# Performance work log

Measured on AMD Instinct MI355X. Metric: run time of the kernel, lower is better.

## Reference

```python
import jax, jax.numpy as jnp
import numpy as np

K = 2            # top-k experts
SCALING = 16.0 / 16.0  # alpha / r


def setup_inputs() -> dict:
    key = jax.random.key(0)
    ks = jax.random.split(key, 7)
    B, T, D, O, E, R = 2, 4096, 2048, 2048, 8, 16
    return {
        "x": jax.random.normal(ks[0], (B, T, D), dtype=jnp.float32),
        "W": jax.random.normal(ks[1], (O, D), dtype=jnp.float32) * (1.0 / np.sqrt(D)),
        "b": jax.random.normal(ks[2], (O,), dtype=jnp.float32) * 0.02,
        "lora_A": jax.random.normal(ks[3], (E, R, D), dtype=jnp.float32) * (1.0 / np.sqrt(D)),
        "lora_B": jax.random.normal(ks[4], (E, O, R), dtype=jnp.float32) * 0.02,
        "gate_w": jax.random.normal(ks[5], (E, D), dtype=jnp.float32) * 0.02,
        "gate_b": jax.random.normal(ks[6], (E,), dtype=jnp.float32) * 0.02,
    }


def reference(x, W, b, lora_A, lora_B, gate_w, gate_b):
    orig_shape = x.shape
    D = orig_shape[-1]
    O = W.shape[0]
    x_flat = x.reshape(-1, D)                                  # [N, D]

    base = x_flat @ W.T + b                                    # [N, O]

    logits = x_flat @ gate_w.T + gate_b                        # [N, E] (eval: no noise)
    topk_logits, topk_idx = jax.lax.top_k(logits, K)           # [N, K]
    gates = jax.nn.softmax(topk_logits, axis=-1)               # [N, K]

    xA = jnp.einsum('nd,erd->ner', x_flat, lora_A)             # [N, E, R]
    delta_all = jnp.einsum('ner,eor->neo', xA, lora_B)         # [N, E, O]

    delta_topk = jnp.take_along_axis(delta_all, topk_idx[:, :, None], axis=1)  # [N, K, O]
    lora_update = jnp.sum(delta_topk * gates[:, :, None], axis=1)              # [N, O]

    out = base + SCALING * lora_update
    return out.reshape(*orig_shape[:-1], O)
```

## Files before the change

### kernel.cpp

```cpp
#include <hip/hip_runtime.h>
#include <hip/hip_bf16.h>
#include <stdint.h>

#define N_ROWS 8192
#define DIM    2048
#define OUTD   2048
#define NEXP   8
#define RNK    16
#define ZCOLS  128
#define KAUG   2176

typedef unsigned short u16;
typedef float  f32x4  __attribute__((ext_vector_type(4)));
typedef __bf16 bf16x8 __attribute__((ext_vector_type(8)));

__device__ __forceinline__ u16 f2bf(float f) {
  unsigned u = __float_as_uint(f);
  return (u16)((u + 0x7fffu + ((u >> 16) & 1u)) >> 16);
}

__global__ __launch_bounds__(256) void k2_weights(
    const float* __restrict__ W, const float* __restrict__ lB,
    const float* __restrict__ lA, u16* __restrict__ waug, u16* __restrict__ ab)
{
  const int t = threadIdx.x;
  const int bid = blockIdx.x;
  if (bid < OUTD) {
    const int o = bid;
    const float* wr = W + (size_t)o * DIM;
    u16* dst = waug + (size_t)o * KAUG;
    #pragma unroll
    for (int i = 0; i < 2; ++i) {
      int c = t * 4 + i * 1024;
      float4 v = *(const float4*)(wr + c);
      ushort4 s; s.x = f2bf(v.x); s.y = f2bf(v.y); s.z = f2bf(v.z); s.w = f2bf(v.w);
      *(ushort4*)(dst + c) = s;
    }
    if (t < ZCOLS) {
      int e = t >> 4, r = t & 15;
      dst[DIM + t] = f2bf(lB[((size_t)e * OUTD + o) * RNK + r]);
    }
  } else {
    const int ar = bid - OUTD;
    const float* src = lA + (size_t)ar * DIM;
    u16* dst = ab + (size_t)ar * DIM;
    #pragma unroll
    for (int i = 0; i < 2; ++i) {
      int c = t * 4 + i * 1024;
      float4 v = *(const float4*)(src + c);
      ushort4 s; s.x = f2bf(v.x); s.y = f2bf(v.y); s.z = f2bf(v.z); s.w = f2bf(v.w);
      *(ushort4*)(dst + c) = s;
    }
  }
}

__global__ __launch_bounds__(256) void kf_fused(
    const float* __restrict__ x, const float* __restrict__ gw,
    const float* __restrict__ gb, const u16* __restrict__ ab,
    u16* __restrict__ xaug)
{
  __shared__ __align__(16) u16 la[8192];
  __shared__ __align__(16) u16 xb[1024];
  __shared__ float4 gates[16];

  const int t    = threadIdx.x;
  const int wave = t >> 6;
  const int lane = t & 63;
  const int r    = t >> 4;
  const int q    = t & 15;
  const size_t row0 = (size_t)blockIdx.x * 16;

  int   lrow[4], lsch[4];
  #pragma unroll
  for (int i = 0; i < 4; ++i) {
    const int g = t + i * 256;
    lrow[i] = g >> 3;
    lsch[i] = (g & 7) ^ (lrow[i] & 7);
  }

  float4 xv, gwv[8];
  xv = *(const float4*)(x + (row0 + r) * DIM + q * 4);
  #pragma unroll
  for (int e = 0; e < NEXP; ++e)
    gwv[e] = *(const float4*)(gw + (size_t)e * DIM + q * 4);

  float ga[NEXP] = {};
  f32x4 acc[2] = {};
  const int nfA = 2 * wave, nfB = 2 * wave + 1;

  for (int c = 0; c < 32; ++c) {
    const int C0 = c * 64;
    #pragma unroll
    for (int i = 0; i < 4; ++i) {
      const char* src = (const char*)(ab + (size_t)lrow[i] * DIM + C0 + lsch[i] * 8);
      __builtin_amdgcn_global_load_lds(
          (__attribute__((address_space(1))) void*)src,
          (__attribute__((address_space(3))) void*)((char*)la + (wave * 64 + i * 256) * 16),
          16, 0, 0);
    }
    __builtin_amdgcn_sched_barrier(0);
    float4 xvn, gwvn[8];
    if (c + 1 < 32) {
      xvn = *(const float4*)(x + (row0 + r) * DIM + C0 + 64 + q * 4);
      #pragma unroll
      for (int e = 0; e < NEXP; ++e)
        gwvn[e] = *(const float4*)(gw + (size_t)e * DIM + C0 + 64 + q * 4);
    }
    __builtin_amdgcn_sched_barrier(0);
    ushort4 s; s.x = f2bf(xv.x); s.y = f2bf(xv.y); s.z = f2bf(xv.z); s.w = f2bf(xv.w);
    *(ushort4*)(xaug + (row0 + r) * KAUG + C0 + q * 4) = s;
    #pragma unroll
    for (int e = 0; e < NEXP; ++e)
      ga[e] += xv.x * gwv[e].x + xv.y * gwv[e].y + xv.z * gwv[e].z + xv.w * gwv[e].w;
    {
      const int ch = q >> 1;
      const int by = r * 128 + ((ch ^ (r & 7)) * 16) + (q & 1) * 8;
      *(ushort4*)((char*)xb + by) = s;
    }
    if (c + 1 < 32) asm volatile("s_waitcnt vmcnt(9)" ::: "memory");
    else            asm volatile("s_waitcnt vmcnt(0)" ::: "memory");
    asm volatile("s_waitcnt lgkmcnt(0)" ::: "memory");
    __builtin_amdgcn_s_barrier();

    #pragma unroll
    for (int ks = 0; ks < 2; ++ks) {
      const int ra  = lane & 15;
      const int pa  = ((ks * 4 + (lane >> 4)) ^ (ra & 7)) * 16;
      bf16x8 avf = *(const bf16x8*)((char*)xb + ra * 128 + pa);
      const int rbA = (lane & 15) + 16 * nfA;
      const int rbB = (lane & 15) + 16 * nfB;
      bf16x8 bvA = *(const bf16x8*)((char*)la + rbA * 128 + (((ks * 4 + (lane >> 4)) ^ (rbA & 7)) * 16));
      bf16x8 bvB = *(const bf16x8*)((char*)la + rbB * 128 + (((ks * 4 + (lane >> 4)) ^ (rbB & 7)) * 16));
      acc[0] = __builtin_amdgcn_mfma_f32_16x16x32_bf16(avf, bvA, acc[0], 0, 0, 0);
      acc[1] = __builtin_amdgcn_mfma_f32_16x16x32_bf16(avf, bvB, acc[1], 0, 0, 0);
    }
    __builtin_amdgcn_s_barrier();
    xv = xvn;
    #pragma unroll
    for (int e = 0; e < NEXP; ++e) gwv[e] = gwvn[e];
  }

  #pragma unroll
  for (int e = 0; e < NEXP; ++e) {
    float v = ga[e];
    v += __shfl_xor(v, 1); v += __shfl_xor(v, 2);
    v += __shfl_xor(v, 4); v += __shfl_xor(v, 8);
    ga[e] = v + gb[e];
  }
  if (q == 0) {
    int e0 = 0; float m0 = ga[0];
    #pragma unroll
    for (int e = 1; e < NEXP; ++e) if (ga[e] > m0) { m0 = ga[e]; e0 = e; }
    int e1 = (e0 == 0) ? 1 : 0; float m1 = ga[e1];
    #pragma unroll
    for (int e = 0; e < NEXP; ++e) if (e != e0 && ga[e] > m1) { m1 = ga[e]; e1 = e; }
    float tt  = expf(m1 - m0);
    float inv = 1.f / (1.f + tt);
    float4 gg; gg.x = inv; gg.y = tt * inv;
    gg.z = __int_as_float(e0); gg.w = __int_as_float(e1);
    gates[r] = gg;
  }
  __syncthreads();

  #pragma unroll
  for (int nfl = 0; nfl < 2; ++nfl) {
    const int e = 2 * wave + nfl;
    const int n = e * 16 + (lane & 15);
    #pragma unroll
    for (int j = 0; j < 4; ++j) {
      const int m = (lane >> 4) * 4 + j;
      float4 gg = gates[m];
      const float g = (e == __float_as_int(gg.z)) ? gg.x
                    : ((e == __float_as_int(gg.w)) ? gg.y : 0.f);
      xaug[(row0 + m) * KAUG + DIM + n] = f2bf(acc[nfl][j] * g);
    }
  }
}

__global__ __launch_bounds__(512, 2) void gemm256_pipe(
    const u16* __restrict__ A, int lda,
    const u16* __restrict__ Bm, int ldb,
    int Ksz, int grid_n,
    float* __restrict__ outF, int ldo, const float* __restrict__ bias)
{
  __shared__ __align__(16) u16 smem[65536];

  const int tid  = threadIdx.x;
  const int wave = tid >> 6;
  const int lane = tid & 63;

  int bid = blockIdx.x;
  const int nwg = gridDim.x;
  if ((nwg & 7) == 0) {
    const int cpx = nwg >> 3;
    bid = (bid & 7) * cpx + (bid >> 3);
  }
  const int tm = bid / grid_n;
  const int tn = bid % grid_n;
  const size_t row0 = (size_t)tm * 256;
  const size_t col0 = (size_t)tn * 256;

  const int l3  = lane >> 3;
  const int sch = ((lane & 7) ^ l3) << 4;
  const char* aSrc = (const char*)(A  + (row0 + (size_t)(wave * 8 + l3)) * lda) + sch;
  const char* bSrc = (const char*)(Bm + (col0 + (size_t)(wave * 8 + l3)) * ldb) + sch;
  const size_t arst = (size_t)lda * 128;
  const size_t brst = (size_t)ldb * 128;
  char* ldsA = (char*)smem + wave * 1024;
  char* ldsB = (char*)smem + 65536 + wave * 1024;

  auto stage = [&](int tt) {
    const size_t ko = (size_t)tt * 128;
    const int    sb = (tt & 1) << 15;
    #pragma unroll
    for (int i = 0; i < 4; ++i)
      __builtin_amdgcn_global_load_lds(
          (__attribute__((address_space(1))) void*)(aSrc + ko + i * arst),
          (__attribute__((address_space(3))) void*)(ldsA + sb + i * 8192), 16, 0, 0);
    #pragma unroll
    for (int i = 0; i < 4; ++i)
      __builtin_amdgcn_global_load_lds(
          (__attribute__((address_space(1))) void*)(bSrc + ko + i * brst),
          (__attribute__((address_space(3))) void*)(ldsB + sb + i * 8192), 16, 0, 0);
  };

  const int wm = wave >> 2, wn = wave & 3;
  const int x0 = ((lane >> 4) ^ (lane & 7)) << 4;
  const int offA0 = wm * 16384 + (lane & 15) * 128 + x0;
  const int offB0 = wn * 8192  + (lane & 15) * 128 + x0;

  f32x4 acc[8][4] = {};

  const int nk = Ksz / 64;
  stage(0); stage(1);

  for (int t = 0; t < nk; ++t) {
    if (t + 1 < nk) asm volatile("s_waitcnt vmcnt(8)" ::: "memory");
    else            asm volatile("s_waitcnt vmcnt(0)" ::: "memory");
    __builtin_amdgcn_s_barrier();
    __builtin_amdgcn_sched_barrier(0);

    const char* sa = (const char*)smem + ((t & 1) << 15);
    const char* sb = (const char*)smem + 65536 + ((t & 1) << 15);

    bf16x8 av0[8], bv0[4], av1[8], bv1[4];
    #pragma unroll
    for (int mf = 0; mf < 8; ++mf) av0[mf] = *(const bf16x8*)(sa + offA0 + mf * 2048);
    #pragma unroll
    for (int nf = 0; nf < 4; ++nf) bv0[nf] = *(const bf16x8*)(sb + offB0 + nf * 2048);
    __builtin_amdgcn_s_setprio(1);
    #pragma unroll
    for (int mf = 0; mf < 8; ++mf)
      #pragma unroll
      for (int nf = 0; nf < 2; ++nf)
        acc[mf][nf] = __builtin_amdgcn_mfma_f32_16x16x32_bf16(
            av0[mf], bv0[nf], acc[mf][nf], 0, 0, 0);
    __builtin_amdgcn_s_setprio(0);
    #pragma unroll
    for (int mf = 0; mf < 8; ++mf) av1[mf] = *(const bf16x8*)(sa + (offA0 ^ 64) + mf * 2048);
    #pragma unroll
    for (int nf = 0; nf < 4; ++nf) bv1[nf] = *(const bf16x8*)(sb + (offB0 ^ 64) + nf * 2048);
    __builtin_amdgcn_s_setprio(1);
    #pragma unroll
    for (int mf = 0; mf < 8; ++mf)
      #pragma unroll
      for (int nf = 2; nf < 4; ++nf)
        acc[mf][nf] = __builtin_amdgcn_mfma_f32_16x16x32_bf16(
            av0[mf], bv0[nf], acc[mf][nf], 0, 0, 0);
    __builtin_amdgcn_s_setprio(0);
    asm volatile("s_waitcnt lgkmcnt(0)" ::: "memory");
    __builtin_amdgcn_s_barrier();
    __builtin_amdgcn_sched_barrier(0);
    if (t + 2 < nk) stage(t + 2);
    __builtin_amdgcn_s_setprio(1);
    #pragma unroll
    for (int mf = 0; mf < 8; ++mf)
      #pragma unroll
      for (int nf = 0; nf < 4; ++nf)
        acc[mf][nf] = __builtin_amdgcn_mfma_f32_16x16x32_bf16(
            av1[mf], bv1[nf], acc[mf][nf], 0, 0, 0);
    __builtin_amdgcn_s_setprio(0);
  }

  #pragma unroll
  for (int nf = 0; nf < 4; ++nf) {
    const size_t c = col0 + wn * 64 + nf * 16 + (lane & 15);
    const float bvv = bias[c];
    #pragma unroll
    for (int mf = 0; mf < 8; ++mf) {
      const size_t rb = row0 + wm * 128 + mf * 16 + ((lane >> 4) << 2);
      #pragma unroll
      for (int j = 0; j < 4; ++j)
        outF[(rb + j) * (size_t)ldo + c] = acc[mf][nf][j] + bvv;
    }
  }
}

extern "C" void kernel_launch(void* const* d_in, const int* in_sizes, int n_in,
                              void* d_out, int out_size, void* d_ws, size_t ws_size,
                              hipStream_t stream) {
  const float* x  = (const float*)d_in[0];
  const float* W  = (const float*)d_in[1];
  const float* b  = (const float*)d_in[2];
  const float* lA = (const float*)d_in[3];
  const float* lB = (const float*)d_in[4];
  const float* gw = (const float*)d_in[5];
  const float* gb = (const float*)d_in[6];
  float* out = (float*)d_out;

  u16* xaug = (u16*)d_ws;
  u16* waug = xaug + (size_t)N_ROWS * KAUG;
  u16* ab   = waug + (size_t)OUTD * KAUG;

  hipLaunchKernelGGL(k2_weights, dim3(OUTD + ZCOLS), dim3(256), 0, stream,
                     W, lB, lA, waug, ab);
  hipLaunchKernelGGL(kf_fused, dim3(N_ROWS / 16), dim3(256), 0, stream,
                     x, gw, gb, ab, xaug);
  hipLaunchKernelGGL(gemm256_pipe,
                     dim3((N_ROWS / 256) * (OUTD / 256)), dim3(512), 0, stream,
                     xaug, KAUG, waug, KAUG, KAUG, OUTD / 256,
                     out, OUTD, b);
}
```

Measured before the change: 120.7 us.

## Restructure GEMM main loop into barrier-phased schedule and double-buffer LoRA-A tiles

The main bf16 GEMM loop is unrolled by two k-steps and split into barrier-separated phases. Each phase interleaves LDS fragment reads with MFMA groups, and the A and B global-to-LDS stages are issued separately so waits cover only what the next step needs. The fused gate/LoRA-A kernel double-buffers its LDS tile, prefetching the next chunk one iteration ahead, but now waits with vmcnt(0) every iteration. The extra barriers add sync overhead, and the full drain in the fused kernel may give back some of the overlap it was meant to add.

```diff
diff --git a/kernel.cpp b/kernel.cpp
--- a/kernel.cpp
+++ b/kernel.cpp
@@ -18,6 +18,10 @@
   unsigned u = __float_as_uint(f);
   return (u16)((u + 0x7fffu + ((u >> 16) & 1u)) >> 16);
 }
+
+#define GLOAD(SRC, DST) __builtin_amdgcn_global_load_lds( \
+    (__attribute__((address_space(1))) void*)(SRC), \
+    (__attribute__((address_space(3))) void*)(DST), 16, 0, 0)
 
 __global__ __launch_bounds__(256) void k2_weights(
     const float* __restrict__ W, const float* __restrict__ lB,
@@ -59,7 +63,7 @@
     const float* __restrict__ gb, const u16* __restrict__ ab,
     u16* __restrict__ xaug)
 {
-  __shared__ __align__(16) u16 la[8192];
+  __shared__ __align__(16) u16 la[2][8192];
   __shared__ __align__(16) u16 xb[1024];
   __shared__ float4 gates[16];
 
@@ -78,11 +82,23 @@
     lsch[i] = (g & 7) ^ (lrow[i] & 7);
   }
 
+  auto stage_la = [&](int c, int h) {
+    const int C0 = c * 64;
+    #pragma unroll
+    for (int i = 0; i < 4; ++i) {
+      const char* src = (const char*)(ab + (size_t)lrow[i] * DIM + C0 + lsch[i] * 8);
+      GLOAD(src, (char*)la[h] + (wave * 64 + i * 256) * 16);
+    }
+  };
+
   float4 xv, gwv[8];
   xv = *(const float4*)(x + (row0 + r) * DIM + q * 4);
   #pragma unroll
   for (int e = 0; e < NEXP; ++e)
     gwv[e] = *(const float4*)(gw + (size_t)e * DIM + q * 4);
+
+  stage_la(0, 0);
+  __builtin_amdgcn_sched_barrier(0);
 
   float ga[NEXP] = {};
   f32x4 acc[2] = {};
@@ -90,14 +106,7 @@
 
   for (int c = 0; c < 32; ++c) {
     const int C0 = c * 64;
-    #pragma unroll
-    for (int i = 0; i < 4; ++i) {
-      const char* src = (const char*)(ab + (size_t)lrow[i] * DIM + C0 + lsch[i] * 8);
-      __builtin_amdgcn_global_load_lds(
-          (__attribute__((address_space(1))) void*)src,
-          (__attribute__((address_space(3))) void*)((char*)la + (wave * 64 + i * 256) * 16),
-          16, 0, 0);
-    }
+    if (c + 1 < 32) stage_la(c + 1, (c + 1) & 1);
     __builtin_amdgcn_sched_barrier(0);
     float4 xvn, gwvn[8];
     if (c + 1 < 32) {
@@ -117,11 +126,11 @@
       const int by = r * 128 + ((ch ^ (r & 7)) * 16) + (q & 1) * 8;
       *(ushort4*)((char*)xb + by) = s;
     }
-    if (c + 1 < 32) asm volatile("s_waitcnt vmcnt(9)" ::: "memory");
-    else            asm volatile("s_waitcnt vmcnt(0)" ::: "memory");
-    asm volatile("s_waitcnt lgkmcnt(0)" ::: "memory");
+    asm volatile("s_waitcnt vmcnt(0) lgkmcnt(0)" ::: "memory");
+    __builtin_amdgcn_sched_barrier(0);
     __builtin_amdgcn_s_barrier();
 
+    const char* lab = (const char*)la[c & 1];
     #pragma unroll
     for (int ks = 0; ks < 2; ++ks) {
       const int ra  = lane & 15;
@@ -129,12 +138,13 @@
       bf16x8 avf = *(const bf16x8*)((char*)xb + ra * 128 + pa);
       const int rbA = (lane & 15) + 16 * nfA;
       const int rbB = (lane & 15) + 16 * nfB;
-      bf16x8 bvA = *(const bf16x8*)((char*)la + rbA * 128 + (((ks * 4 + (lane >> 4)) ^ (rbA & 7)) * 16));
-      bf16x8 bvB = *(const bf16x8*)((char*)la + rbB * 128 + (((ks * 4 + (lane >> 4)) ^ (rbB & 7)) * 16));
+      bf16x8 bvA = *(const bf16x8*)(lab + rbA * 128 + (((ks * 4 + (lane >> 4)) ^ (rbA & 7)) * 16));
+      bf16x8 bvB = *(const bf16x8*)(lab + rbB * 128 + (((ks * 4 + (lane >> 4)) ^ (rbB & 7)) * 16));
       acc[0] = __builtin_amdgcn_mfma_f32_16x16x32_bf16(avf, bvA, acc[0], 0, 0, 0);
       acc[1] = __builtin_amdgcn_mfma_f32_16x16x32_bf16(avf, bvB, acc[1], 0, 0, 0);
     }
     __builtin_amdgcn_s_barrier();
+    __builtin_amdgcn_sched_barrier(0);
     xv = xvn;
     #pragma unroll
     for (int e = 0; e < NEXP; ++e) gwv[e] = gwvn[e];
@@ -176,6 +186,26 @@
     }
   }
 }
+
+#define LGKM0 do { asm volatile("s_waitcnt lgkmcnt(0)" ::: "memory"); \
+                   __builtin_amdgcn_sched_barrier(0); } while (0)
+#define PH_END do { __builtin_amdgcn_s_barrier(); \
+                    __builtin_amdgcn_sched_barrier(0); } while (0)
+#define MFMA_G(AV, BV, NFB) do { \
+  __builtin_amdgcn_s_setprio(1); \
+  _Pragma("unroll") \
+  for (int mf = 0; mf < 8; ++mf) { \
+    acc[mf][NFB]     = __builtin_amdgcn_mfma_f32_16x16x32_bf16(AV[mf], BV[NFB],     acc[mf][NFB],     0, 0, 0); \
+    acc[mf][NFB + 1] = __builtin_amdgcn_mfma_f32_16x16x32_bf16(AV[mf], BV[NFB + 1], acc[mf][NFB + 1], 0, 0, 0); \
+  } \
+  __builtin_amdgcn_s_setprio(0); \
+} while (0)
+#define RD_A(DST, BASE, XOR) do { _Pragma("unroll") \
+  for (int mf = 0; mf < 8; ++mf) \
+    DST[mf] = *(const bf16x8*)((BASE) + ((offA0) ^ (XOR)) + mf * 2048); } while (0)
+#define RD_B(DST, BASE, XOR) do { _Pragma("unroll") \
+  for (int nf = 0; nf < 4; ++nf) \
+    DST[nf] = *(const bf16x8*)((BASE) + ((offB0) ^ (XOR)) + nf * 2048); } while (0)
 
 __global__ __launch_bounds__(512, 2) void gemm256_pipe(
     const u16* __restrict__ A, int lda,
@@ -209,19 +239,19 @@
   char* ldsA = (char*)smem + wave * 1024;
   char* ldsB = (char*)smem + 65536 + wave * 1024;
 
-  auto stage = [&](int tt) {
+  auto stageA = [&](int tt) {
     const size_t ko = (size_t)tt * 128;
     const int    sb = (tt & 1) << 15;
     #pragma unroll
     for (int i = 0; i < 4; ++i)
-      __builtin_amdgcn_global_load_lds(
-          (__attribute__((address_space(1))) void*)(aSrc + ko + i * arst),
-          (__attribute__((address_space(3))) void*)(ldsA + sb + i * 8192), 16, 0, 0);
+      GLOAD(aSrc + ko + i * arst, ldsA + sb + i * 8192);
+  };
+  auto stageB = [&](int tt) {
+    const size_t ko = (size_t)tt * 128;
+    const int    sb = (tt & 1) << 15;
     #pragma unroll
     for (int i = 0; i < 4; ++i)
-      __builtin_amdgcn_global_load_lds(
-          (__attribute__((address_space(1))) void*)(bSrc + ko + i * brst),
-          (__attribute__((address_space(3))) void*)(ldsB + sb + i * 8192), 16, 0, 0);
+      GLOAD(bSrc + ko + i * brst, ldsB + sb + i * 8192);
   };
 
   const int wm = wave >> 2, wn = wave & 3;
@@ -231,55 +261,57 @@
 
   f32x4 acc[8][4] = {};
 
-  const int nk = Ksz / 64;
-  stage(0); stage(1);
-
-  for (int t = 0; t < nk; ++t) {
-    if (t + 1 < nk) asm volatile("s_waitcnt vmcnt(8)" ::: "memory");
-    else            asm volatile("s_waitcnt vmcnt(0)" ::: "memory");
+  const int nk    = Ksz / 64;
+  const int niter = nk / 2;
+
+  stageA(0); stageB(0); stageA(1); stageB(1);
+  asm volatile("s_waitcnt vmcnt(8)" ::: "memory");
+  __builtin_amdgcn_s_barrier();
+  __builtin_amdgcn_sched_barrier(0);
+
+  for (int it = 0; it < niter; ++it) {
+    const int T = 2 * it;
+    const bool more = (it + 1 < niter);
+    const char* sa0 = (const char*)smem;
+    const char* sb0 = (const char*)smem + 65536;
+    const char* sa1 = (const char*)smem + 32768;
+    const char* sb1 = (const char*)smem + 98304;
+    bf16x8 av0[8], bv0[4], av1[8], bv1[4];
+
+    RD_A(av0, sa0, 0); RD_B(bv0, sb0, 0);
+    __builtin_amdgcn_s_barrier(); LGKM0;
+    MFMA_G(av0, bv0, 0); PH_END;
+    RD_A(av1, sa0, 64);
+    __builtin_amdgcn_s_barrier(); LGKM0;
+    MFMA_G(av0, bv0, 2); PH_END;
+    RD_B(bv1, sb0, 64);
+    if (more) stageA(T + 2);
+    __builtin_amdgcn_s_barrier(); LGKM0;
+    MFMA_G(av1, bv1, 0); PH_END;
+    if (more) asm volatile("s_waitcnt vmcnt(4)" ::: "memory");
+    else      asm volatile("s_waitcnt vmcnt(0)" ::: "memory");
+    __builtin_amdgcn_sched_barrier(0);
+    if (more) stageB(T + 2);
     __builtin_amdgcn_s_barrier();
     __builtin_amdgcn_sched_barrier(0);
-
-    const char* sa = (const char*)smem + ((t & 1) << 15);
-    const char* sb = (const char*)smem + 65536 + ((t & 1) << 15);
-
-    bf16x8 av0[8], bv0[4], av1[8], bv1[4];
-    #pragma unroll
-    for (int mf = 0; mf < 8; ++mf) av0[mf] = *(const bf16x8*)(sa + offA0 + mf * 2048);
-    #pragma unroll
-    for (int nf = 0; nf < 4; ++nf) bv0[nf] = *(const bf16x8*)(sb + offB0 + nf * 2048);
-    __builtin_amdgcn_s_setprio(1);
-    #pragma unroll
-    for (int mf = 0; mf < 8; ++mf)
-      #pragma unroll
-      for (int nf = 0; nf < 2; ++nf)
-        acc[mf][nf] = __builtin_amdgcn_mfma_f32_16x16x32_bf16(
-            av0[mf], bv0[nf], acc[mf][nf], 0, 0, 0);
-    __builtin_amdgcn_s_setprio(0);
-    #pragma unroll
-    for (int mf = 0; mf < 8; ++mf) av1[mf] = *(const bf16x8*)(sa + (offA0 ^ 64) + mf * 2048);
-    #pragma unroll
-    for (int nf = 0; nf < 4; ++nf) bv1[nf] = *(const bf16x8*)(sb + (offB0 ^ 64) + nf * 2048);
-    __builtin_amdgcn_s_setprio(1);
-    #pragma unroll
-    for (int mf = 0; mf < 8; ++mf)
-      #pragma unroll
-      for (int nf = 2; nf < 4; ++nf)
-        acc[mf][nf] = __builtin_amdgcn_mfma_f32_16x16x32_bf16(
-            av0[mf], bv0[nf], acc[mf][nf], 0, 0, 0);
-    __builtin_amdgcn_s_setprio(0);
-    asm volatile("s_waitcnt lgkmcnt(0)" ::: "memory");
+    MFMA_G(av1, bv1, 2); PH_END;
+    RD_A(av0, sa1, 0); RD_B(bv0, sb1, 0);
+    __builtin_amdgcn_s_barrier(); LGKM0;
+    MFMA_G(av0, bv0, 0); PH_END;
+    RD_A(av1, sa1, 64);
+    __builtin_amdgcn_s_barrier(); LGKM0;
+    MFMA_G(av0, bv0, 2); PH_END;
+    RD_B(bv1, sb1, 64);
+    if (more) stageA(T + 3);
+    __builtin_amdgcn_s_barrier(); LGKM0;
+    MFMA_G(av1, bv1, 0); PH_END;
+    if (more) asm volatile("s_waitcnt vmcnt(4)" ::: "memory");
+    else      asm volatile("s_waitcnt vmcnt(0)" ::: "memory");
+    __builtin_amdgcn_sched_barrier(0);
+    if (more) stageB(T + 3);
     __builtin_amdgcn_s_barrier();
     __builtin_amdgcn_sched_barrier(0);
-    if (t + 2 < nk) stage(t + 2);
-    __builtin_amdgcn_s_setprio(1);
-    #pragma unroll
-    for (int mf = 0; mf < 8; ++mf)
-      #pragma unroll
-      for (int nf = 0; nf < 4; ++nf)
-        acc[mf][nf] = __builtin_amdgcn_mfma_f32_16x16x32_bf16(
-            av1[mf], bv1[nf], acc[mf][nf], 0, 0, 0);
-    __builtin_amdgcn_s_setprio(0);
+    MFMA_G(av1, bv1, 2); PH_END;
   }
 
   #pragma unroll
```

Result: slower. 126.8 us (+5.1%).

## Overlap W bf16 conversion with gating pass and double-buffer LoRA-A tiles

Applied to the files above, without the earlier changes.

The lora_A conversion moves into its own small kernel. The W/lora_B to bf16 conversion is folded into the fused gating/xA kernel as extra blocks, so weight packing runs concurrently with the activation pass instead of as a separate serial launch. Inside the fused kernel, the LoRA-A LDS tile is now double-buffered and prefetched one chunk ahead, with adjusted waitcnt values. This raises LDS use per block and lets heterogeneous blocks share one launch, so scheduling may be uneven.

```diff
diff --git a/kernel.cpp b/kernel.cpp
--- a/kernel.cpp
+++ b/kernel.cpp
@@ -19,14 +19,37 @@
   return (u16)((u + 0x7fffu + ((u >> 16) & 1u)) >> 16);
 }
 
-__global__ __launch_bounds__(256) void k2_weights(
+#define GLOAD(SRC, DST) __builtin_amdgcn_global_load_lds( \
+    (__attribute__((address_space(1))) void*)(SRC), \
+    (__attribute__((address_space(3))) void*)(DST), 16, 0, 0)
+
+__global__ __launch_bounds__(256) void k2a_lora(
+    const float* __restrict__ lA, u16* __restrict__ ab)
+{
+  const int t  = threadIdx.x;
+  const int ar = blockIdx.x;
+  const float* src = lA + (size_t)ar * DIM;
+  u16* dst = ab + (size_t)ar * DIM;
+  #pragma unroll
+  for (int i = 0; i < 2; ++i) {
+    int c = t * 4 + i * 1024;
+    float4 v = *(const float4*)(src + c);
+    ushort4 s; s.x = f2bf(v.x); s.y = f2bf(v.y); s.z = f2bf(v.z); s.w = f2bf(v.w);
+    *(ushort4*)(dst + c) = s;
+  }
+}
+
+__global__ __launch_bounds__(256) void kfw_fused(
+    const float* __restrict__ x, const float* __restrict__ gw,
+    const float* __restrict__ gb, const u16* __restrict__ ab,
+    u16* __restrict__ xaug,
     const float* __restrict__ W, const float* __restrict__ lB,
-    const float* __restrict__ lA, u16* __restrict__ waug, u16* __restrict__ ab)
+    u16* __restrict__ waug)
 {
   const int t = threadIdx.x;
-  const int bid = blockIdx.x;
-  if (bid < OUTD) {
-    const int o = bid;
+
+  if (blockIdx.x >= 512) {
+    const int o = blockIdx.x - 512;
     const float* wr = W + (size_t)o * DIM;
     u16* dst = waug + (size_t)o * KAUG;
     #pragma unroll
@@ -40,30 +63,13 @@
       int e = t >> 4, r = t & 15;
       dst[DIM + t] = f2bf(lB[((size_t)e * OUTD + o) * RNK + r]);
     }
-  } else {
-    const int ar = bid - OUTD;
-    const float* src = lA + (size_t)ar * DIM;
-    u16* dst = ab + (size_t)ar * DIM;
-    #pragma unroll
-    for (int i = 0; i < 2; ++i) {
-      int c = t * 4 + i * 1024;
-      float4 v = *(const float4*)(src + c);
-      ushort4 s; s.x = f2bf(v.x); s.y = f2bf(v.y); s.z = f2bf(v.z); s.w = f2bf(v.w);
-      *(ushort4*)(dst + c) = s;
-    }
-  }
-}
-
-__global__ __launch_bounds__(256) void kf_fused(
-    const float* __restrict__ x, const float* __restrict__ gw,
-    const float* __restrict__ gb, const u16* __restrict__ ab,
-    u16* __restrict__ xaug)
-{
-  __shared__ __align__(16) u16 la[8192];
+    return;
+  }
+
+  __shared__ __align__(16) u16 la[2][8192];
   __shared__ __align__(16) u16 xb[1024];
   __shared__ float4 gates[16];
 
-  const int t    = threadIdx.x;
   const int wave = t >> 6;
   const int lane = t & 63;
   const int r    = t >> 4;
@@ -78,6 +84,18 @@
     lsch[i] = (g & 7) ^ (lrow[i] & 7);
   }
 
+  auto stage_la = [&](int c, int h) {
+    const int C0 = c * 64;
+    #pragma unroll
+    for (int i = 0; i < 4; ++i) {
+      const char* src = (const char*)(ab + (size_t)lrow[i] * DIM + C0 + lsch[i] * 8);
+      GLOAD(src, (char*)la[h] + (wave * 64 + i * 256) * 16);
+    }
+  };
+
+  stage_la(0, 0);
+  __builtin_amdgcn_sched_barrier(0);
+
   float4 xv, gwv[8];
   xv = *(const float4*)(x + (row0 + r) * DIM + q * 4);
   #pragma unroll
@@ -90,14 +108,7 @@
 
   for (int c = 0; c < 32; ++c) {
     const int C0 = c * 64;
-    #pragma unroll
-    for (int i = 0; i < 4; ++i) {
-      const char* src = (const char*)(ab + (size_t)lrow[i] * DIM + C0 + lsch[i] * 8);
-      __builtin_amdgcn_global_load_lds(
-          (__attribute__((address_space(1))) void*)src,
-          (__attribute__((address_space(3))) void*)((char*)la + (wave * 64 + i * 256) * 16),
-          16, 0, 0);
-    }
+    if (c + 1 < 32) stage_la(c + 1, (c + 1) & 1);
     __builtin_amdgcn_sched_barrier(0);
     float4 xvn, gwvn[8];
     if (c + 1 < 32) {
@@ -117,11 +128,12 @@
       const int by = r * 128 + ((ch ^ (r & 7)) * 16) + (q & 1) * 8;
       *(ushort4*)((char*)xb + by) = s;
     }
-    if (c + 1 < 32) asm volatile("s_waitcnt vmcnt(9)" ::: "memory");
-    else            asm volatile("s_waitcnt vmcnt(0)" ::: "memory");
-    asm volatile("s_waitcnt lgkmcnt(0)" ::: "memory");
+    if (c + 1 < 32) asm volatile("s_waitcnt vmcnt(22) lgkmcnt(0)" ::: "memory");
+    else            asm volatile("s_waitcnt vmcnt(0) lgkmcnt(0)" ::: "memory");
+    __builtin_amdgcn_sched_barrier(0);
     __builtin_amdgcn_s_barrier();
 
+    const char* lab = (const char*)la[c & 1];
     #pragma unroll
     for (int ks = 0; ks < 2; ++ks) {
       const int ra  = lane & 15;
@@ -129,12 +141,13 @@
       bf16x8 avf = *(const bf16x8*)((char*)xb + ra * 128 + pa);
       const int rbA = (lane & 15) + 16 * nfA;
       const int rbB = (lane & 15) + 16 * nfB;
-      bf16x8 bvA = *(const bf16x8*)((char*)la + rbA * 128 + (((ks * 4 + (lane >> 4)) ^ (rbA & 7)) * 16));
-      bf16x8 bvB = *(const bf16x8*)((char*)la + rbB * 128 + (((ks * 4 + (lane >> 4)) ^ (rbB & 7)) * 16));
+      bf16x8 bvA = *(const bf16x8*)(lab + rbA * 128 + (((ks * 4 + (lane >> 4)) ^ (rbA & 7)) * 16));
+      bf16x8 bvB = *(const bf16x8*)(lab + rbB * 128 + (((ks * 4 + (lane >> 4)) ^ (rbB & 7)) * 16));
       acc[0] = __builtin_amdgcn_mfma_f32_16x16x32_bf16(avf, bvA, acc[0], 0, 0, 0);
       acc[1] = __builtin_amdgcn_mfma_f32_16x16x32_bf16(avf, bvB, acc[1], 0, 0, 0);
     }
     __builtin_amdgcn_s_barrier();
+    __builtin_amdgcn_sched_barrier(0);
     xv = xvn;
     #pragma unroll
     for (int e = 0; e < NEXP; ++e) gwv[e] = gwvn[e];
@@ -214,14 +227,10 @@
     const int    sb = (tt & 1) << 15;
     #pragma unroll
     for (int i = 0; i < 4; ++i)
-      __builtin_amdgcn_global_load_lds(
-          (__attribute__((address_space(1))) void*)(aSrc + ko + i * arst),
-          (__attribute__((address_space(3))) void*)(ldsA + sb + i * 8192), 16, 0, 0);
+      GLOAD(aSrc + ko + i * arst, ldsA + sb + i * 8192);
     #pragma unroll
     for (int i = 0; i < 4; ++i)
-      __builtin_amdgcn_global_load_lds(
-          (__attribute__((address_space(1))) void*)(bSrc + ko + i * brst),
-          (__attribute__((address_space(3))) void*)(ldsB + sb + i * 8192), 16, 0, 0);
+      GLOAD(bSrc + ko + i * brst, ldsB + sb + i * 8192);
   };
 
   const int wm = wave >> 2, wn = wave & 3;
@@ -312,10 +321,9 @@
   u16* waug = xaug + (size_t)N_ROWS * KAUG;
   u16* ab   = waug + (size_t)OUTD * KAUG;
 
-  hipLaunchKernelGGL(k2_weights, dim3(OUTD + ZCOLS), dim3(256), 0, stream,
-                     W, lB, lA, waug, ab);
-  hipLaunchKernelGGL(kf_fused, dim3(N_ROWS / 16), dim3(256), 0, stream,
-                     x, gw, gb, ab, xaug);
+  hipLaunchKernelGGL(k2a_lora, dim3(ZCOLS), dim3(256), 0, stream, lA, ab);
+  hipLaunchKernelGGL(kfw_fused, dim3(512 + OUTD), dim3(256), 0, stream,
+                     x, gw, gb, ab, xaug, W, lB, waug);
   hipLaunchKernelGGL(gemm256_pipe,
                      dim3((N_ROWS / 256) * (OUTD / 256)), dim3(512), 0, stream,
                      xaug, KAUG, waug, KAUG, KAUG, OUTD / 256,
```

Result: faster. 116.8 us (-3.2%).
